# Kernel optimization log

Hardware: AMD Instinct MI355X
Metric: run time of the kernel (lower is better)

## Reference

```python
import jax, jax.numpy as jnp
import numpy as np

N_NODES = 50000
N_EDGES = 800000
D_FEAT = 64          # per-node feature dim
HIDDEN = 128         # fc1 output dim; fc1 input = 2*D_FEAT


def setup_inputs() -> dict:
    key = jax.random.key(0)
    k1, k2, k3 = jax.random.split(key, 3)
    x = jax.random.normal(k1, (N_NODES, D_FEAT), dtype=jnp.float32)
    edge_index = jax.random.randint(k2, (2, N_EDGES), 0, N_NODES, dtype=jnp.int64)
    # fc1: Linear(2*D_FEAT, HIDDEN); torch Linear weight is [out, in]
    W = jax.random.normal(k3, (HIDDEN, 2 * D_FEAT), dtype=jnp.float32) * (1.0 / np.sqrt(2 * D_FEAT))
    b = jnp.zeros((HIDDEN,), dtype=jnp.float32)
    return {"x": x, "edge_index": edge_index, "W": W, "b": b}


def reference(x, edge_index, W, b):
    # Gather source-node features along edges, sum-scatter to destinations.
    src, dst = edge_index[0], edge_index[1]
    gathered = x[src]  # [E, D_FEAT] -- dominant memory traffic
    neigh = jax.ops.segment_sum(gathered, dst, num_segments=x.shape[0])  # [N, D_FEAT]
    # Concat self features with aggregated neighbor features, then Linear+ReLU.
    h = jnp.concatenate([x, neigh], axis=-1)          # [N, 2*D_FEAT]
    out = jax.nn.relu(h @ W.T + b)                    # [N, HIDDEN]
    return out
```

## Files before the change

### kernel.cpp

```cpp
#include <hip/hip_runtime.h>

#define N_NODES 50000
#define N_EDGES 800000
#define DFEAT 64
#define HID 128
#define NBKT 782
#define NSEG 391
#define SEGW 16
#define CAP_S 1536
#define NSTR 66

#define XB2 1563
#define WB2 8
#define EB2 391

typedef __bf16 bf16x8 __attribute__((ext_vector_type(8)));
typedef float f32x4 __attribute__((ext_vector_type(4)));

__device__ inline unsigned short f2bf(float f) {
  unsigned u = __float_as_uint(f);
  return (unsigned short)((u + 0x7FFFu + ((u >> 16) & 1u)) >> 16);
}
__device__ inline float bf2f(unsigned short h) {
  return __uint_as_float(((unsigned)h) << 16);
}

__global__ __launch_bounds__(512) void k_prep(const float* __restrict__ x,
                                              const float* __restrict__ W,
                                              const int* __restrict__ ei,
                                              unsigned short* __restrict__ xb,
                                              unsigned short* __restrict__ Wb,
                                              unsigned int* __restrict__ coarse) {
  int bid = blockIdx.x;
  const int tid = threadIdx.x;
  if (bid < XB2) {
    int t = bid * 512 + tid;
    if (t < N_NODES * DFEAT / 4) {
      float4 v = *(const float4*)&x[t * 4];
      ushort4 o = {f2bf(v.x), f2bf(v.y), f2bf(v.z), f2bf(v.w)};
      *(ushort4*)&xb[t * 4] = o;
    }
    return;
  }
  bid -= XB2;
  if (bid < WB2) {
    int t = bid * 512 + tid;
    float4 v = *(const float4*)&W[t * 4];
    ushort4 o = {f2bf(v.x), f2bf(v.y), f2bf(v.z), f2bf(v.w)};
    *(ushort4*)&Wb[t * 4] = o;
    return;
  }
  bid -= WB2;
  __shared__ int lcnt[NBKT];
  for (int i = tid; i < NBKT; i += 512) lcnt[i] = 0;
  __syncthreads();

  int e0 = (bid * 512 + tid) * 4;
  if (e0 < N_EDGES) {
    int4 s4 = *(const int4*)&ei[e0];
    int4 d4 = *(const int4*)&ei[N_EDGES + e0];
    int ss[4] = {s4.x, s4.y, s4.z, s4.w};
    int dd[4] = {d4.x, d4.y, d4.z, d4.w};
#pragma unroll
    for (int i = 0; i < 4; ++i) {
      int bkt = dd[i] >> 6;
      int rank = atomicAdd(&lcnt[bkt], 1);
      if (rank < SEGW - 1)
        coarse[(size_t)bkt * (NSEG * SEGW) + bid * SEGW + 1 + rank] =
            ((unsigned)dd[i] << 16) | (unsigned)ss[i];
    }
  }
  __syncthreads();
  for (int i = tid; i < NBKT; i += 512) {
    int c = lcnt[i];
    coarse[(size_t)i * (NSEG * SEGW) + bid * SEGW] =
        (unsigned)(c < SEGW - 1 ? c : SEGW - 1);
  }
}

__global__ __launch_bounds__(1024) void k_gnn(const unsigned short* __restrict__ xb,
                                              const unsigned short* __restrict__ Wb,
                                              const unsigned int* __restrict__ coarse,
                                              const float* __restrict__ bv,
                                              float* __restrict__ out) {
  __shared__ unsigned int q[CAP_S];
  __shared__ unsigned int sq[CAP_S];
  __shared__ unsigned int ns_u[32 * NSTR];
  __shared__ int scnt[NSEG];
  __shared__ int lcnt[64];
  __shared__ int lbase[65];
  __shared__ int qn;

  const int tid = threadIdx.x;
  const int b = blockIdx.x;
  const int nb = b * 64;
  const unsigned int* base = coarse + (size_t)b * (NSEG * SEGW);

  if (tid < 64) lcnt[tid] = 0;
  if (tid == 0) qn = 0;
  for (int i = tid; i < NSEG; i += 1024) {
    int c = (int)base[i * SEGW];
    scnt[i] = c < SEGW - 1 ? c : SEGW - 1;
  }
  __syncthreads();

  const int NU4 = NSEG * SEGW / 4;
  for (int i = tid; i < NU4; i += 1024) {
    uint4 w = ((const uint4*)base)[i];
    int seg = i >> 2;
    int wi = (i & 3) * 4;
    int cnt = scnt[seg];
    unsigned e[4] = {w.x, w.y, w.z, w.w};
#pragma unroll
    for (int k = 0; k < 4; ++k) {
      int widx = wi + k;
      if (widx >= 1 && widx <= cnt) {
        int pos = atomicAdd(&qn, 1);
        if (pos < CAP_S) q[pos] = e[k] & 0x003fffffu;
      }
    }
  }
  __syncthreads();

  int cnt = qn < CAP_S ? qn : CAP_S;

  int myrank[2], myidx[2], nloc = 0;
  for (int i = tid; i < cnt; i += 1024) {
    int rel = (int)(q[i] >> 16);
    myrank[nloc] = atomicAdd(&lcnt[rel], 1);
    myidx[nloc] = i;
    ++nloc;
  }
  __syncthreads();
  if (tid < 64) {
    int v = lcnt[tid];
    int inc = v;
#pragma unroll
    for (int o = 1; o < 64; o <<= 1) {
      int u = __shfl_up(inc, o);
      if (tid >= o) inc += u;
    }
    lbase[tid] = inc - v;
    if (tid == 63) lbase[64] = inc;
  }
  __syncthreads();
  for (int k = 0; k < nloc; ++k) {
    unsigned e = q[myidx[k]];
    sq[lbase[e >> 16] + myrank[k]] = e;
  }
  __syncthreads();

  const int wave = tid >> 6;
  const int lane = tid & 63;
  const int eslot = lane >> 4;
  const int c = lane & 15;
  const uint2* xu2 = (const uint2*)xb;

#pragma unroll
  for (int i2 = 0; i2 < 4; ++i2) {
    int n = wave * 4 + i2;
    int beg = lbase[n], end = lbase[n + 1];
    float f0 = 0.f, f1 = 0.f, f2 = 0.f, f3 = 0.f;
    float g0 = 0.f, g1 = 0.f, g2 = 0.f, g3 = 0.f;
    int j = beg + eslot;
    for (; j + 4 < end; j += 8) {
      unsigned e0 = sq[j], e1 = sq[j + 4];
      uint2 v0 = xu2[(e0 & 0xffffu) * 16 + c];
      uint2 v1 = xu2[(e1 & 0xffffu) * 16 + c];
      f0 += bf2f((unsigned short)(v0.x & 0xffffu)); f1 += bf2f((unsigned short)(v0.x >> 16));
      f2 += bf2f((unsigned short)(v0.y & 0xffffu)); f3 += bf2f((unsigned short)(v0.y >> 16));
      g0 += bf2f((unsigned short)(v1.x & 0xffffu)); g1 += bf2f((unsigned short)(v1.x >> 16));
      g2 += bf2f((unsigned short)(v1.y & 0xffffu)); g3 += bf2f((unsigned short)(v1.y >> 16));
    }
    for (; j < end; j += 4) {
      unsigned e = sq[j];
      uint2 v = xu2[(e & 0xffffu) * 16 + c];
      f0 += bf2f((unsigned short)(v.x & 0xffffu)); f1 += bf2f((unsigned short)(v.x >> 16));
      f2 += bf2f((unsigned short)(v.y & 0xffffu)); f3 += bf2f((unsigned short)(v.y >> 16));
    }
    f0 += g0; f1 += g1; f2 += g2; f3 += g3;
    f0 += __shfl_xor(f0, 16); f0 += __shfl_xor(f0, 32);
    f1 += __shfl_xor(f1, 16); f1 += __shfl_xor(f1, 32);
    f2 += __shfl_xor(f2, 16); f2 += __shfl_xor(f2, 32);
    f3 += __shfl_xor(f3, 16); f3 += __shfl_xor(f3, 32);
    if (eslot == 0) {
      ns_u[(2 * c) * NSTR + n] = (unsigned)f2bf(f0) | ((unsigned)f2bf(f1) << 16);
      ns_u[(2 * c + 1) * NSTR + n] = (unsigned)f2bf(f2) | ((unsigned)f2bf(f3) << 16);
    }
  }
  __syncthreads();

  const int g = wave & 3;
  const int o = wave >> 2;
  const int l15 = lane & 15;
  const int quad = lane >> 4;
  const int node0 = nb + g * 16;

  int anode = node0 + l15;
  if (anode >= N_NODES) anode = N_NODES - 1;
  const unsigned short* hx = xb + (size_t)anode * DFEAT;

  bf16x8 fa0 = *(const bf16x8*)(hx + quad * 8);
  bf16x8 fa1 = *(const bf16x8*)(hx + 32 + quad * 8);
  bf16x8 fa2, fa3;
  {
    int m = g * 16 + l15;
    union { unsigned u[4]; bf16x8 v; } c2, c3;
#pragma unroll
    for (int i = 0; i < 4; ++i) {
      c2.u[i] = ns_u[(quad * 4 + i) * NSTR + m];
      c3.u[i] = ns_u[(16 + quad * 4 + i) * NSTR + m];
    }
    fa2 = c2.v;
    fa3 = c3.v;
  }

  f32x4 accr[2];
#pragma unroll
  for (int t = 0; t < 2; ++t) accr[t] = (f32x4){0.f, 0.f, 0.f, 0.f};

#pragma unroll
  for (int t = 0; t < 2; ++t) {
    int nt = o * 2 + t;
    const unsigned short* wr = Wb + (size_t)(nt * 16 + l15) * (2 * DFEAT) + quad * 8;
    bf16x8 b0 = *(const bf16x8*)(wr);
    bf16x8 b1 = *(const bf16x8*)(wr + 32);
    bf16x8 b2 = *(const bf16x8*)(wr + 64);
    bf16x8 b3 = *(const bf16x8*)(wr + 96);
    accr[t] = __builtin_amdgcn_mfma_f32_16x16x32_bf16(fa0, b0, accr[t], 0, 0, 0);
    accr[t] = __builtin_amdgcn_mfma_f32_16x16x32_bf16(fa1, b1, accr[t], 0, 0, 0);
    accr[t] = __builtin_amdgcn_mfma_f32_16x16x32_bf16(fa2, b2, accr[t], 0, 0, 0);
    accr[t] = __builtin_amdgcn_mfma_f32_16x16x32_bf16(fa3, b3, accr[t], 0, 0, 0);
  }

#pragma unroll
  for (int t = 0; t < 2; ++t) {
    int nt = o * 2 + t;
    float bias = bv[nt * 16 + l15];
#pragma unroll
    for (int r = 0; r < 4; ++r) {
      int node = node0 + quad * 4 + r;
      if (node < N_NODES) {
        float v = accr[t][r] + bias;
        out[(size_t)node * HID + nt * 16 + l15] = v > 0.f ? v : 0.f;
      }
    }
  }
}

extern "C" void kernel_launch(void* const* d_in, const int* in_sizes, int n_in,
                              void* d_out, int out_size, void* d_ws, size_t ws_size,
                              hipStream_t stream) {
  const float* x = (const float*)d_in[0];
  const int* ei = (const int*)d_in[1];
  const float* W = (const float*)d_in[2];
  const float* b = (const float*)d_in[3];
  float* out = (float*)d_out;

  char* ws = (char*)d_ws;
  unsigned int* coarse = (unsigned int*)ws;   ws += (size_t)NBKT * NSEG * SEGW * 4;
  unsigned short* xb   = (unsigned short*)ws; ws += (size_t)N_NODES * DFEAT * 2;
  unsigned short* Wb   = (unsigned short*)ws; ws += (size_t)HID * 2 * DFEAT * 2;

  k_prep<<<XB2 + WB2 + EB2, 512, 0, stream>>>(x, W, ei, xb, Wb, coarse);
  k_gnn<<<NBKT, 1024, 0, stream>>>(xb, Wb, coarse, b, out);
}
```

Before: 126.7 us.

## Use 16-byte neighbor gathers and a prefix-scan queue build in GNN kernel

The neighbor gather now has each lane load 16 bytes (8 bf16 features) instead of 8, with 8 edge slots per wave, and converts bf16 pairs with packed intrinsics. This halves the number of load instructions per row and widens each memory request. The edge queue is now filled from a block-wide prefix scan over segment counts, one thread per segment, instead of a shared atomic counter. The scan costs about 18 block barriers and serial per-thread copies, which may offset the removed atomic contention.

```diff
diff --git a/kernel.cpp b/kernel.cpp
--- a/kernel.cpp
+++ b/kernel.cpp
@@ -1,4 +1,5 @@
 #include <hip/hip_runtime.h>
+#include <hip/hip_bf16.h>
 
 #define N_NODES 50000
 #define N_EDGES 800000
@@ -21,8 +22,9 @@
   unsigned u = __float_as_uint(f);
   return (unsigned short)((u + 0x7FFFu + ((u >> 16) & 1u)) >> 16);
 }
-__device__ inline float bf2f(unsigned short h) {
-  return __uint_as_float(((unsigned)h) << 16);
+__device__ inline float2 bf2x2(unsigned v) {
+  __hip_bfloat162 h = *reinterpret_cast<const __hip_bfloat162*>(&v);
+  return __bfloat1622float2(h);
 }
 
 __global__ __launch_bounds__(512) void k_prep(const float* __restrict__ x,
@@ -87,9 +89,9 @@
   __shared__ unsigned int sq[CAP_S];
   __shared__ unsigned int ns_u[32 * NSTR];
   __shared__ int scnt[NSEG];
+  __shared__ int sc[512];
   __shared__ int lcnt[64];
   __shared__ int lbase[65];
-  __shared__ int qn;
 
   const int tid = threadIdx.x;
   const int b = blockIdx.x;
@@ -97,32 +99,32 @@
   const unsigned int* base = coarse + (size_t)b * (NSEG * SEGW);
 
   if (tid < 64) lcnt[tid] = 0;
-  if (tid == 0) qn = 0;
-  for (int i = tid; i < NSEG; i += 1024) {
-    int c = (int)base[i * SEGW];
-    scnt[i] = c < SEGW - 1 ? c : SEGW - 1;
-  }
-  __syncthreads();
-
-  const int NU4 = NSEG * SEGW / 4;
-  for (int i = tid; i < NU4; i += 1024) {
-    uint4 w = ((const uint4*)base)[i];
-    int seg = i >> 2;
-    int wi = (i & 3) * 4;
-    int cnt = scnt[seg];
-    unsigned e[4] = {w.x, w.y, w.z, w.w};
-#pragma unroll
-    for (int k = 0; k < 4; ++k) {
-      int widx = wi + k;
-      if (widx >= 1 && widx <= cnt) {
-        int pos = atomicAdd(&qn, 1);
-        if (pos < CAP_S) q[pos] = e[k] & 0x003fffffu;
-      }
-    }
-  }
-  __syncthreads();
-
-  int cnt = qn < CAP_S ? qn : CAP_S;
+  if (tid < NSEG) {
+    int c = (int)base[tid * SEGW];
+    scnt[tid] = c < SEGW - 1 ? c : SEGW - 1;
+  }
+  __syncthreads();
+  if (tid < 512) sc[tid] = (tid < NSEG) ? scnt[tid] : 0;
+  __syncthreads();
+#pragma unroll
+  for (int o = 1; o < 512; o <<= 1) {
+    int u = 0;
+    if (tid < 512 && tid >= o) u = sc[tid - o];
+    __syncthreads();
+    if (tid < 512) sc[tid] += u;
+    __syncthreads();
+  }
+  if (tid < NSEG) {
+    int c = scnt[tid];
+    int qs = sc[tid] - c;
+    for (int k = 0; k < c; ++k) {
+      int pos = qs + k;
+      if (pos < CAP_S) q[pos] = base[tid * SEGW + 1 + k] & 0x003fffffu;
+    }
+  }
+  __syncthreads();
+  int cnt = sc[511];
+  cnt = cnt < CAP_S ? cnt : CAP_S;
 
   int myrank[2], myidx[2], nloc = 0;
   for (int i = tid; i < cnt; i += 1024) {
@@ -152,40 +154,54 @@
 
   const int wave = tid >> 6;
   const int lane = tid & 63;
-  const int eslot = lane >> 4;
-  const int c = lane & 15;
-  const uint2* xu2 = (const uint2*)xb;
+  const int eslot = lane >> 3;
+  const int c = lane & 7;
+  const uint4* xu4 = (const uint4*)xb;
 
 #pragma unroll
   for (int i2 = 0; i2 < 4; ++i2) {
     int n = wave * 4 + i2;
     int beg = lbase[n], end = lbase[n + 1];
-    float f0 = 0.f, f1 = 0.f, f2 = 0.f, f3 = 0.f;
-    float g0 = 0.f, g1 = 0.f, g2 = 0.f, g3 = 0.f;
+    float2 a0 = {0.f, 0.f}, a1 = {0.f, 0.f}, a2 = {0.f, 0.f}, a3 = {0.f, 0.f};
+    float2 b0 = {0.f, 0.f}, b1 = {0.f, 0.f}, b2 = {0.f, 0.f}, b3 = {0.f, 0.f};
     int j = beg + eslot;
-    for (; j + 4 < end; j += 8) {
-      unsigned e0 = sq[j], e1 = sq[j + 4];
-      uint2 v0 = xu2[(e0 & 0xffffu) * 16 + c];
-      uint2 v1 = xu2[(e1 & 0xffffu) * 16 + c];
-      f0 += bf2f((unsigned short)(v0.x & 0xffffu)); f1 += bf2f((unsigned short)(v0.x >> 16));
-      f2 += bf2f((unsigned short)(v0.y & 0xffffu)); f3 += bf2f((unsigned short)(v0.y >> 16));
-      g0 += bf2f((unsigned short)(v1.x & 0xffffu)); g1 += bf2f((unsigned short)(v1.x >> 16));
-      g2 += bf2f((unsigned short)(v1.y & 0xffffu)); g3 += bf2f((unsigned short)(v1.y >> 16));
-    }
-    for (; j < end; j += 4) {
+    for (; j + 8 < end; j += 16) {
+      unsigned e0 = sq[j], e1 = sq[j + 8];
+      uint4 v0 = xu4[(e0 & 0xffffu) * 8 + c];
+      uint4 v1 = xu4[(e1 & 0xffffu) * 8 + c];
+      float2 p;
+      p = bf2x2(v0.x); a0.x += p.x; a0.y += p.y;
+      p = bf2x2(v0.y); a1.x += p.x; a1.y += p.y;
+      p = bf2x2(v0.z); a2.x += p.x; a2.y += p.y;
+      p = bf2x2(v0.w); a3.x += p.x; a3.y += p.y;
+      p = bf2x2(v1.x); b0.x += p.x; b0.y += p.y;
+      p = bf2x2(v1.y); b1.x += p.x; b1.y += p.y;
+      p = bf2x2(v1.z); b2.x += p.x; b2.y += p.y;
+      p = bf2x2(v1.w); b3.x += p.x; b3.y += p.y;
+    }
+    for (; j < end; j += 8) {
       unsigned e = sq[j];
-      uint2 v = xu2[(e & 0xffffu) * 16 + c];
-      f0 += bf2f((unsigned short)(v.x & 0xffffu)); f1 += bf2f((unsigned short)(v.x >> 16));
-      f2 += bf2f((unsigned short)(v.y & 0xffffu)); f3 += bf2f((unsigned short)(v.y >> 16));
-    }
-    f0 += g0; f1 += g1; f2 += g2; f3 += g3;
-    f0 += __shfl_xor(f0, 16); f0 += __shfl_xor(f0, 32);
-    f1 += __shfl_xor(f1, 16); f1 += __shfl_xor(f1, 32);
-    f2 += __shfl_xor(f2, 16); f2 += __shfl_xor(f2, 32);
-    f3 += __shfl_xor(f3, 16); f3 += __shfl_xor(f3, 32);
+      uint4 v = xu4[(e & 0xffffu) * 8 + c];
+      float2 p;
+      p = bf2x2(v.x); a0.x += p.x; a0.y += p.y;
+      p = bf2x2(v.y); a1.x += p.x; a1.y += p.y;
+      p = bf2x2(v.z); a2.x += p.x; a2.y += p.y;
+      p = bf2x2(v.w); a3.x += p.x; a3.y += p.y;
+    }
+    a0.x += b0.x; a0.y += b0.y; a1.x += b1.x; a1.y += b1.y;
+    a2.x += b2.x; a2.y += b2.y; a3.x += b3.x; a3.y += b3.y;
+    float f[8] = {a0.x, a0.y, a1.x, a1.y, a2.x, a2.y, a3.x, a3.y};
+#pragma unroll
+    for (int k = 0; k < 8; ++k) {
+      f[k] += __shfl_xor(f[k], 8);
+      f[k] += __shfl_xor(f[k], 16);
+      f[k] += __shfl_xor(f[k], 32);
+    }
     if (eslot == 0) {
-      ns_u[(2 * c) * NSTR + n] = (unsigned)f2bf(f0) | ((unsigned)f2bf(f1) << 16);
-      ns_u[(2 * c + 1) * NSTR + n] = (unsigned)f2bf(f2) | ((unsigned)f2bf(f3) << 16);
+#pragma unroll
+      for (int i = 0; i < 4; ++i)
+        ns_u[(4 * c + i) * NSTR + n] =
+            (unsigned)f2bf(f[2 * i]) | ((unsigned)f2bf(f[2 * i + 1]) << 16);
     }
   }
   __syncthreads();
@@ -223,14 +239,14 @@
   for (int t = 0; t < 2; ++t) {
     int nt = o * 2 + t;
     const unsigned short* wr = Wb + (size_t)(nt * 16 + l15) * (2 * DFEAT) + quad * 8;
-    bf16x8 b0 = *(const bf16x8*)(wr);
-    bf16x8 b1 = *(const bf16x8*)(wr + 32);
-    bf16x8 b2 = *(const bf16x8*)(wr + 64);
-    bf16x8 b3 = *(const bf16x8*)(wr + 96);
-    accr[t] = __builtin_amdgcn_mfma_f32_16x16x32_bf16(fa0, b0, accr[t], 0, 0, 0);
-    accr[t] = __builtin_amdgcn_mfma_f32_16x16x32_bf16(fa1, b1, accr[t], 0, 0, 0);
-    accr[t] = __builtin_amdgcn_mfma_f32_16x16x32_bf16(fa2, b2, accr[t], 0, 0, 0);
-    accr[t] = __builtin_amdgcn_mfma_f32_16x16x32_bf16(fa3, b3, accr[t], 0, 0, 0);
+    bf16x8 w0 = *(const bf16x8*)(wr);
+    bf16x8 w1 = *(const bf16x8*)(wr + 32);
+    bf16x8 w2 = *(const bf16x8*)(wr + 64);
+    bf16x8 w3 = *(const bf16x8*)(wr + 96);
+    accr[t] = __builtin_amdgcn_mfma_f32_16x16x32_bf16(fa0, w0, accr[t], 0, 0, 0);
+    accr[t] = __builtin_amdgcn_mfma_f32_16x16x32_bf16(fa1, w1, accr[t], 0, 0, 0);
+    accr[t] = __builtin_amdgcn_mfma_f32_16x16x32_bf16(fa2, w2, accr[t], 0, 0, 0);
+    accr[t] = __builtin_amdgcn_mfma_f32_16x16x32_bf16(fa3, w3, accr[t], 0, 0, 0);
   }
 
 #pragma unroll
```

Result: slower. 139.1 us (+9.8%).
